# Optimization experiments

Hardware: AMD Instinct MI355X
Metric: run time of the kernel (lower is better)

## Reference

```python
import jax, jax.numpy as jnp
import numpy as np

E = 1024   # embed_dim
H = 16     # num_heads
NQ = 8     # ffn_dim == n_qubits
B, S = 2, 2048


def setup_inputs() -> dict:
    key = jax.random.key(0)
    ks = jax.random.split(key, 8)
    g = lambda k, sh, sc=1.0: jax.random.normal(k, sh, jnp.float32) * sc
    return {
        "x": g(ks[0], (B, S, E)),
        "w_qkv": g(ks[1], (3 * E, E), 0.02),      # nn.Linear(E, 3E, bias=False).weight
        "w_comb": g(ks[2], (E, E), 0.02),          # combine Linear weight
        "b_comb": jnp.zeros((E,), jnp.float32),
        "gamma1": jnp.ones((E,), jnp.float32),     # norm1
        "beta1": jnp.zeros((E,), jnp.float32),
        "gamma2": jnp.ones((E,), jnp.float32),     # norm2
        "beta2": jnp.zeros((E,), jnp.float32),
        "theta": g(ks[3], (NQ,)),                  # trainable RY angles
        "w1": g(ks[4], (1, NQ), 0.3),              # linear1 weight [1, n_qubits]
        "b1": jnp.zeros((1,), jnp.float32),
    }


def _layernorm(x, g, b, eps=1e-5):
    m = jnp.mean(x, axis=-1, keepdims=True)
    v = jnp.var(x, axis=-1, keepdims=True)
    return (x - m) * jax.lax.rsqrt(v + eps) * g + b


def reference(x, w_qkv, w_comb, b_comb, gamma1, beta1, gamma2, beta2, theta, w1, b1):
    Bx, Sx, Em = x.shape
    dk = Em // H
    # ---- attention ----
    qkv = (x @ w_qkv.T).reshape(Bx, Sx, 3, H, dk)
    q = jnp.transpose(qkv[:, :, 0], (0, 2, 1, 3))  # [B,H,S,dk]
    k = jnp.transpose(qkv[:, :, 1], (0, 2, 1, 3))
    v = jnp.transpose(qkv[:, :, 2], (0, 2, 1, 3))
    scores = jnp.einsum('bhqd,bhkd->bhqk', q, k) / jnp.sqrt(jnp.float32(dk))
    probs = jax.nn.softmax(scores, axis=-1)        # dropout = identity (eval)
    out = jnp.einsum('bhqk,bhkd->bhqd', probs, v)
    out = jnp.transpose(out, (0, 2, 1, 3)).reshape(Bx, Sx, Em)
    attn = out @ w_comb.T + b_comb
    x1 = _layernorm(x + attn, gamma1, beta1)
    # ---- quantum FFN: RX(x_i) encode, RY(theta_i), <Z_i> = cos(theta_i)*cos(x_i) ----
    z = jnp.cos(x1[..., :theta.shape[0]]) * jnp.cos(theta)  # [B,S,NQ]
    ffn = z @ w1.T + b1                                      # [B,S,1], broadcasts
    return _layernorm(x1 + ffn, gamma2, beta2)
```

## Files before the change

### kernel.cpp

```cpp
#include <hip/hip_runtime.h>
#include <hip/hip_bf16.h>
#include <math.h>

typedef __bf16 bf16;
typedef bf16 bf16x8 __attribute__((ext_vector_type(8)));
typedef float f32x4 __attribute__((ext_vector_type(4)));
typedef unsigned int u32;

#define EMB 1024
#define NH 16
#define DK 64
#define SEQ 2048
#define NB 2
#define NTOK (NB*SEQ)

#define QSCALE 0.18033688011112043f

#if defined(__has_builtin)
#if __has_builtin(__builtin_amdgcn_exp2f)
#define EXP2(x) __builtin_amdgcn_exp2f(x)
#else
#define EXP2(x) exp2f(x)
#endif
#else
#define EXP2(x) exp2f(x)
#endif

__device__ __forceinline__ void gl_lds16(const void* g, void* l) {
    __builtin_amdgcn_global_load_lds(
        (const __attribute__((address_space(1))) u32*)g,
        (__attribute__((address_space(3))) u32*)l, 16, 0, 0);
}

#define SWZ(row, colblk) (((row)*64) + ((((colblk) ^ ((row)&7)))*8))

#define PSTR 72

__global__ __launch_bounds__(256) void convert3(
    const float* __restrict__ s0, const float* __restrict__ s1,
    const float* __restrict__ s2,
    bf16* __restrict__ d0, bf16* __restrict__ d1, bf16* __restrict__ d2)
{
    const float* src; bf16* dst; int n;
    switch (blockIdx.y) {
        case 0:  src = s0; dst = d0; n = NTOK*EMB;  break;
        case 1:  src = s1; dst = d1; n = 3*EMB*EMB; break;
        default: src = s2; dst = d2; n = EMB*EMB;   break;
    }
    int i = (blockIdx.x * 256 + threadIdx.x) * 4;
    if (i + 3 < n) {
        float4 v = *(const float4*)(src + i);
        dst[i+0] = (bf16)v.x; dst[i+1] = (bf16)v.y;
        dst[i+2] = (bf16)v.z; dst[i+3] = (bf16)v.w;
    }
}

template<int MODE, int BM>
__global__ __launch_bounds__(256) void gemm_bt(
    const bf16* __restrict__ Aa, const bf16* __restrict__ Bb,
    bf16* __restrict__ qb, bf16* __restrict__ kb, bf16* __restrict__ vtb,
    float* __restrict__ outc, int Kdim)
{
    constexpr int MI = BM / 32;
    __shared__ __align__(16) bf16 At[BM*64];
    __shared__ __align__(16) bf16 Bt[128*64];
    const int tid  = threadIdx.x;
    const int w    = tid >> 6, lane = tid & 63;
    const int quad = lane >> 4, l15 = lane & 15;
    const int wr   = w >> 1,   wc  = w & 1;
    const int m0 = blockIdx.y * BM, n0 = blockIdx.x * 128;
    const int lrow = lane >> 3;
    const int lswz = ((lane & 7) ^ lrow) * 8;

    f32x4 acc[MI][4] = {};

    for (int k0 = 0; k0 < Kdim; k0 += 64) {
        __syncthreads();
        for (int i = 0; i < MI; ++i) {
            int r = w*(BM/4) + i*8 + lrow;
            gl_lds16(Aa + (size_t)(m0 + r)*Kdim + k0 + lswz, At + (w*(BM/4) + i*8)*64);
        }
        for (int i = 0; i < 4; ++i) {
            int r = w*32 + i*8 + lrow;
            gl_lds16(Bb + (size_t)(n0 + r)*Kdim + k0 + lswz, Bt + (w*32 + i*8)*64);
        }
        __syncthreads();
        for (int kk = 0; kk < 2; ++kk) {
            bf16x8 a[MI], b[4];
            for (int i = 0; i < MI; ++i) {
                int row = wr*(BM/2) + i*16 + l15;
                a[i] = *(const bf16x8*)(At + SWZ(row, 4*kk + quad));
            }
            for (int j = 0; j < 4; ++j) {
                int row = wc*64 + j*16 + l15;
                b[j] = *(const bf16x8*)(Bt + SWZ(row, 4*kk + quad));
            }
            for (int i = 0; i < MI; ++i)
                for (int j = 0; j < 4; ++j)
                    acc[i][j] = __builtin_amdgcn_mfma_f32_16x16x32_bf16(a[i], b[j], acc[i][j], 0, 0, 0);
        }
    }

    for (int i = 0; i < MI; ++i) for (int j = 0; j < 4; ++j) {
        int rb  = m0 + wr*(BM/2) + i*16 + quad*4;
        int col = n0 + wc*64 + j*16 + l15;
        if (MODE == 0) {
            int c = col >> 10, h = (col >> 6) & 15, d = col & 63;
            int b_ = rb >> 11, s = rb & 2047;
            int bh = b_*NH + h;
            if (c == 2) {
                bf16 tmp[4] __attribute__((aligned(8)));
                for (int r = 0; r < 4; ++r) tmp[r] = (bf16)acc[i][j][r];
                *(ushort4*)(vtb + ((size_t)bh*DK + d)*SEQ + s) = *(ushort4*)tmp;
            } else if (c == 0) {
                for (int r = 0; r < 4; ++r)
                    qb[((size_t)bh*SEQ + s + r)*DK + d] = (bf16)(acc[i][j][r] * QSCALE);
            } else {
                for (int r = 0; r < 4; ++r)
                    kb[((size_t)bh*SEQ + s + r)*DK + d] = (bf16)acc[i][j][r];
            }
        } else {
            for (int r = 0; r < 4; ++r)
                outc[(size_t)(rb + r)*EMB + col] = acc[i][j][r];
        }
    }
}

__global__ __launch_bounds__(512) void attn_kernel(
    const bf16* __restrict__ q, const bf16* __restrict__ k,
    const bf16* __restrict__ vt, bf16* __restrict__ out)
{
    __shared__ __align__(16) bf16 QP[8*16*PSTR];
    __shared__ __align__(16) bf16 Kt0[64*64];
    __shared__ __align__(16) bf16 Kt1[64*64];
    __shared__ __align__(16) bf16 Vt0[64*64];
    __shared__ __align__(16) bf16 Vt1[64*64];

    const int tid  = threadIdx.x;
    const int w    = tid >> 6, lane = tid & 63;
    const int quad = lane >> 4, l15 = lane & 15;
    const int bh = blockIdx.y, qt = blockIdx.x;
    const int lrow = lane >> 3;
    const int lswz = ((lane & 7) ^ lrow) * 8;

    for (int i = 0; i < 2; ++i) {
        int r = w*16 + i*8 + lrow;
        gl_lds16(q + ((size_t)bh*SEQ + qt*128 + r)*DK + lswz, QP + (w*16 + i*8)*64);
    }
    asm volatile("s_waitcnt vmcnt(0)" ::: "memory");

    bf16x8 qf[2];
    for (int kk = 0; kk < 2; ++kk)
        qf[kk] = *(const bf16x8*)(QP + SWZ(w*16 + l15, 4*kk + quad));

    bf16* Pw = QP + w * 16 * PSTR;

    f32x4 O[4] = {};
    float psum[4] = {};

    auto stage_kv = [&](int kt, bf16* Kb, bf16* Vb) {
        int r = w*8 + lrow;
        gl_lds16(k  + ((size_t)bh*SEQ + kt*64 + r)*DK + lswz, Kb + (w*8)*64);
        gl_lds16(vt + ((size_t)bh*DK + r)*SEQ + kt*64 + lswz, Vb + (w*8)*64);
    };

    auto compute = [&](const bf16* Kb, const bf16* Vb) {
        f32x4 sc[4] = {};
        for (int kk = 0; kk < 2; ++kk)
            for (int j = 0; j < 4; ++j) {
                bf16x8 b = *(const bf16x8*)(Kb + SWZ(j*16 + l15, 4*kk + quad));
                sc[j] = __builtin_amdgcn_mfma_f32_16x16x32_bf16(qf[kk], b, sc[j], 0, 0, 0);
            }
        for (int j = 0; j < 4; ++j)
            for (int r = 0; r < 4; ++r) {
                float p = EXP2(sc[j][r]);
                psum[r] += p;
                Pw[(quad*4 + r)*PSTR + j*16 + l15] = (bf16)p;
            }
        asm volatile("s_waitcnt lgkmcnt(0)" ::: "memory");
        for (int kk = 0; kk < 2; ++kk) {
            bf16x8 vb[4];
            for (int j = 0; j < 4; ++j)
                vb[j] = *(const bf16x8*)(Vb + SWZ(j*16 + l15, 4*kk + quad));
            bf16x8 a = *(const bf16x8*)(Pw + l15*PSTR + kk*32 + quad*8);
            for (int j = 0; j < 4; ++j)
                O[j] = __builtin_amdgcn_mfma_f32_16x16x32_bf16(a, vb[j], O[j], 0, 0, 0);
        }
    };

    stage_kv(0, Kt0, Vt0);
    for (int kt2 = 0; kt2 < SEQ/128; ++kt2) {
        __syncthreads();
        stage_kv(2*kt2 + 1, Kt1, Vt1);
        compute(Kt0, Vt0);
        __syncthreads();
        if (kt2 + 1 < SEQ/128)
            stage_kv(2*kt2 + 2, Kt0, Vt0);
        compute(Kt1, Vt1);
    }

    for (int r = 0; r < 4; ++r) {
        float s = psum[r];
        for (int m = 1; m < 16; m <<= 1) s += __shfl_xor(s, m, 64);
        psum[r] = 1.f / s;
    }

    const int b_ = bh >> 4, h = bh & 15;
    for (int j = 0; j < 4; ++j)
        for (int r = 0; r < 4; ++r) {
            int t   = b_*SEQ + qt*128 + w*16 + quad*4 + r;
            int col = h*DK + j*16 + l15;
            out[(size_t)t*EMB + col] = (bf16)(O[j][r] * psum[r]);
        }
}

__global__ __launch_bounds__(256) void ln_kernel(
    const float* __restrict__ x, const float* __restrict__ comb,
    const float* __restrict__ bcomb,
    const float* __restrict__ g1, const float* __restrict__ be1,
    const float* __restrict__ g2, const float* __restrict__ be2,
    const float* __restrict__ theta, const float* __restrict__ w1v,
    const float* __restrict__ b1v, float* __restrict__ out)
{
    const int t = blockIdx.x, tid = threadIdx.x;
    __shared__ float red[8];
    __shared__ float fp2[2];
    const int e0 = tid*4;

    float4 xv = *(const float4*)(x    + (size_t)t*EMB + e0);
    float4 cv = *(const float4*)(comb + (size_t)t*EMB + e0);
    float4 bv = *(const float4*)(bcomb + e0);
    float r[4] = { xv.x + cv.x + bv.x, xv.y + cv.y + bv.y,
                   xv.z + cv.z + bv.z, xv.w + cv.w + bv.w };

    float s = 0.f, ss = 0.f;
    for (int i = 0; i < 4; ++i) { s += r[i]; ss += r[i]*r[i]; }
    for (int m = 1; m < 64; m <<= 1) { s += __shfl_xor(s, m, 64); ss += __shfl_xor(ss, m, 64); }
    if ((tid & 63) == 0) { red[(tid>>6)*2] = s; red[(tid>>6)*2+1] = ss; }
    __syncthreads();
    s  = red[0] + red[2] + red[4] + red[6];
    ss = red[1] + red[3] + red[5] + red[7];
    float mean = s * (1.f/1024.f);
    float var  = ss * (1.f/1024.f) - mean*mean;
    float inv  = rsqrtf(var + 1e-5f);
    float x1[4];
    for (int i = 0; i < 4; ++i) {
        int e = e0 + i;
        x1[i] = (r[i] - mean)*inv*g1[e] + be1[e];
    }
    __syncthreads();
    if (e0 < 8) {
        float pf = 0.f;
        for (int i = 0; i < 4; ++i) {
            int e = e0 + i;
            pf += cosf(x1[i]) * cosf(theta[e]) * w1v[e];
        }
        fp2[tid] = pf;
    }
    __syncthreads();
    float f = fp2[0] + fp2[1] + b1v[0];

    float s2 = 0.f, ss2 = 0.f;
    for (int i = 0; i < 4; ++i) { float v2 = x1[i] + f; s2 += v2; ss2 += v2*v2; }
    for (int m = 1; m < 64; m <<= 1) { s2 += __shfl_xor(s2, m, 64); ss2 += __shfl_xor(ss2, m, 64); }
    if ((tid & 63) == 0) { red[(tid>>6)*2] = s2; red[(tid>>6)*2+1] = ss2; }
    __syncthreads();
    s2  = red[0] + red[2] + red[4] + red[6];
    ss2 = red[1] + red[3] + red[5] + red[7];
    float mean2 = s2 * (1.f/1024.f);
    float var2  = ss2 * (1.f/1024.f) - mean2*mean2;
    float inv2  = rsqrtf(var2 + 1e-5f);
    float4 ov;
    ov.x = ((x1[0] + f) - mean2)*inv2*g2[e0+0] + be2[e0+0];
    ov.y = ((x1[1] + f) - mean2)*inv2*g2[e0+1] + be2[e0+1];
    ov.z = ((x1[2] + f) - mean2)*inv2*g2[e0+2] + be2[e0+2];
    ov.w = ((x1[3] + f) - mean2)*inv2*g2[e0+3] + be2[e0+3];
    *(float4*)(out + (size_t)t*EMB + e0) = ov;
}

extern "C" void kernel_launch(void* const* d_in, const int* in_sizes, int n_in,
                              void* d_out, int out_size, void* d_ws, size_t ws_size,
                              hipStream_t stream)
{
    const float* x      = (const float*)d_in[0];
    const float* w_qkv  = (const float*)d_in[1];
    const float* w_comb = (const float*)d_in[2];
    const float* b_comb = (const float*)d_in[3];
    const float* g1     = (const float*)d_in[4];
    const float* be1    = (const float*)d_in[5];
    const float* g2     = (const float*)d_in[6];
    const float* be2    = (const float*)d_in[7];
    const float* theta  = (const float*)d_in[8];
    const float* w1v    = (const float*)d_in[9];
    const float* b1v    = (const float*)d_in[10];
    float* out = (float*)d_out;

    char* ws = (char*)d_ws;
    bf16*  xb     = (bf16*)(ws);
    bf16*  wqkvb  = (bf16*)(ws + ( 8u<<20));
    bf16*  wcombb = (bf16*)(ws + (14u<<20));
    bf16*  qb     = (bf16*)(ws + (16u<<20));
    bf16*  kb     = (bf16*)(ws + (24u<<20));
    bf16*  vtb    = (bf16*)(ws + (32u<<20));
    bf16*  attn   = (bf16*)(ws + (40u<<20));
    float* comb   = (float*)(ws + (16u<<20));

    convert3<<<dim3(4096, 3), 256, 0, stream>>>(x, w_qkv, w_comb, xb, wqkvb, wcombb);

    gemm_bt<0,128><<<dim3(3*EMB/128, NTOK/128), 256, 0, stream>>>(
        xb, wqkvb, qb, kb, vtb, nullptr, EMB);
    attn_kernel<<<dim3(SEQ/128, NB*NH), 512, 0, stream>>>(qb, kb, vtb, attn);
    gemm_bt<1,64><<<dim3(EMB/128, NTOK/64), 256, 0, stream>>>(
        attn, wcombb, nullptr, nullptr, nullptr, comb, EMB);
    ln_kernel<<<NTOK, 256, 0, stream>>>(x, comb, b_comb, g1, be1, g2, be2,
                                        theta, w1v, b1v, out);
}
```

Baseline: 217.5 us.

## Transpose QK^T MFMA, vectorize P stores, add XCD remap and MFMA priority

The attention score MFMA now takes K as the A operand and Q as B, so each lane holds one query's scores. That lets P be written to LDS as packed 4-element vectors instead of scalar stores, and the row sum collapses to a single scalar reduced with fewer shuffles. Separately, both GEMM and attention grids get an XCD-aware block remapping to improve L2 locality, and s_setprio brackets around the MFMA loops. The remap assumes the block count is divisible by 8.

Result: faster. 202.4 us (-7.0%).

```diff
diff --git a/kernel.cpp b/kernel.cpp
--- a/kernel.cpp
+++ b/kernel.cpp
@@ -4,6 +4,7 @@
 
 typedef __bf16 bf16;
 typedef bf16 bf16x8 __attribute__((ext_vector_type(8)));
+typedef bf16 bf16x4 __attribute__((ext_vector_type(4)));
 typedef float f32x4 __attribute__((ext_vector_type(4)));
 typedef unsigned int u32;
 
@@ -36,6 +37,16 @@
 
 #define PSTR 72
 
+__device__ __forceinline__ void xcd_remap(int gx, int* bx, int* by) {
+    int gy  = gridDim.y;
+    int nwg = gx * gy;
+    int wg  = *by * gx + *bx;
+    int per = nwg >> 3;
+    int s   = (wg & 7) * per + (wg >> 3);
+    *bx = s % gx;
+    *by = s / gx;
+}
+
 __global__ __launch_bounds__(256) void convert3(
     const float* __restrict__ s0, const float* __restrict__ s1,
     const float* __restrict__ s2,
@@ -68,7 +79,9 @@
     const int w    = tid >> 6, lane = tid & 63;
     const int quad = lane >> 4, l15 = lane & 15;
     const int wr   = w >> 1,   wc  = w & 1;
-    const int m0 = blockIdx.y * BM, n0 = blockIdx.x * 128;
+    int bx = blockIdx.x, by = blockIdx.y;
+    xcd_remap(gridDim.x, &bx, &by);
+    const int m0 = by * BM, n0 = bx * 128;
     const int lrow = lane >> 3;
     const int lswz = ((lane & 7) ^ lrow) * 8;
 
@@ -95,9 +108,11 @@
                 int row = wc*64 + j*16 + l15;
                 b[j] = *(const bf16x8*)(Bt + SWZ(row, 4*kk + quad));
             }
+            __builtin_amdgcn_s_setprio(1);
             for (int i = 0; i < MI; ++i)
                 for (int j = 0; j < 4; ++j)
                     acc[i][j] = __builtin_amdgcn_mfma_f32_16x16x32_bf16(a[i], b[j], acc[i][j], 0, 0, 0);
+            __builtin_amdgcn_s_setprio(0);
         }
     }
 
@@ -139,7 +154,8 @@
     const int tid  = threadIdx.x;
     const int w    = tid >> 6, lane = tid & 63;
     const int quad = lane >> 4, l15 = lane & 15;
-    const int bh = blockIdx.y, qt = blockIdx.x;
+    int qt = blockIdx.x, bh = blockIdx.y;
+    xcd_remap(gridDim.x, &qt, &bh);
     const int lrow = lane >> 3;
     const int lswz = ((lane & 7) ^ lrow) * 8;
 
@@ -156,7 +172,7 @@
     bf16* Pw = QP + w * 16 * PSTR;
 
     f32x4 O[4] = {};
-    float psum[4] = {};
+    float psum = 0.f;
 
     auto stage_kv = [&](int kt, bf16* Kb, bf16* Vb) {
         int r = w*8 + lrow;
@@ -166,25 +182,34 @@
 
     auto compute = [&](const bf16* Kb, const bf16* Vb) {
         f32x4 sc[4] = {};
-        for (int kk = 0; kk < 2; ++kk)
-            for (int j = 0; j < 4; ++j) {
-                bf16x8 b = *(const bf16x8*)(Kb + SWZ(j*16 + l15, 4*kk + quad));
-                sc[j] = __builtin_amdgcn_mfma_f32_16x16x32_bf16(qf[kk], b, sc[j], 0, 0, 0);
-            }
-        for (int j = 0; j < 4; ++j)
+        for (int kk = 0; kk < 2; ++kk) {
+            bf16x8 kf[4];
+            for (int j = 0; j < 4; ++j)
+                kf[j] = *(const bf16x8*)(Kb + SWZ(j*16 + l15, 4*kk + quad));
+            __builtin_amdgcn_s_setprio(1);
+            for (int j = 0; j < 4; ++j)
+                sc[j] = __builtin_amdgcn_mfma_f32_16x16x32_bf16(kf[j], qf[kk], sc[j], 0, 0, 0);
+            __builtin_amdgcn_s_setprio(0);
+        }
+        for (int j = 0; j < 4; ++j) {
+            bf16x4 pk;
             for (int r = 0; r < 4; ++r) {
                 float p = EXP2(sc[j][r]);
-                psum[r] += p;
-                Pw[(quad*4 + r)*PSTR + j*16 + l15] = (bf16)p;
+                psum += p;
+                pk[r] = (bf16)p;
             }
+            *(bf16x4*)(Pw + l15*PSTR + j*16 + quad*4) = pk;
+        }
         asm volatile("s_waitcnt lgkmcnt(0)" ::: "memory");
         for (int kk = 0; kk < 2; ++kk) {
             bf16x8 vb[4];
             for (int j = 0; j < 4; ++j)
                 vb[j] = *(const bf16x8*)(Vb + SWZ(j*16 + l15, 4*kk + quad));
             bf16x8 a = *(const bf16x8*)(Pw + l15*PSTR + kk*32 + quad*8);
+            __builtin_amdgcn_s_setprio(1);
             for (int j = 0; j < 4; ++j)
                 O[j] = __builtin_amdgcn_mfma_f32_16x16x32_bf16(a, vb[j], O[j], 0, 0, 0);
+            __builtin_amdgcn_s_setprio(0);
         }
     };
 
@@ -199,18 +224,19 @@
         compute(Kt1, Vt1);
     }
 
-    for (int r = 0; r < 4; ++r) {
-        float s = psum[r];
-        for (int m = 1; m < 16; m <<= 1) s += __shfl_xor(s, m, 64);
-        psum[r] = 1.f / s;
-    }
+    float s = psum;
+    s += __shfl_xor(s, 16, 64);
+    s += __shfl_xor(s, 32, 64);
+    float inv[4];
+    for (int r = 0; r < 4; ++r)
+        inv[r] = 1.f / __shfl(s, quad*4 + r, 64);
 
     const int b_ = bh >> 4, h = bh & 15;
     for (int j = 0; j < 4; ++j)
         for (int r = 0; r < 4; ++r) {
             int t   = b_*SEQ + qt*128 + w*16 + quad*4 + r;
             int col = h*DK + j*16 + l15;
-            out[(size_t)t*EMB + col] = (bf16)(O[j][r] * psum[r]);
+            out[(size_t)t*EMB + col] = (bf16)(O[j][r] * inv[r]);
         }
 }
 
```
